# Optimization experiments

Hardware: AMD Instinct MI355X
Metric: run time of the kernel (lower is better)

## Reference

```python
import jax, jax.numpy as jnp
import numpy as np
from jax import lax

B, C, H, W = 4, 256, 32, 32   # latent: NCHW, C == codebook embed dim
N_CODES = 16384


def setup_inputs() -> dict:
    key = jax.random.key(0)
    k1, k2, k3 = jax.random.split(key, 3)
    latent = jax.random.normal(k1, (B, C, H, W), jnp.float32)
    codebook = jax.random.normal(k2, (N_CODES, C), jnp.float32)
    dec_w = jax.random.normal(k3, (3, C, 3, 3), jnp.float32) * 0.02
    dec_b = jnp.zeros((3,), jnp.float32)
    return {"latent": latent, "codebook": codebook, "dec_w": dec_w, "dec_b": dec_b}


def vector_quantize(x, codebook):
    # x: [B,H,W,D], codebook: [N,D]. Squared-L2 nearest neighbor + gather,
    # straight-through gradient (replace_grad(x_q, x)).
    d = ((x * x).sum(-1, keepdims=True)
         - 2.0 * jnp.einsum('bhwd,nd->bhwn', x, codebook)
         + (codebook * codebook).sum(-1))          # [B,H,W,N]
    idx = jnp.argmin(d, axis=-1)                    # [B,H,W]
    x_q = codebook[idx]                             # gather -> [B,H,W,D]
    return x + lax.stop_gradient(x_q - x)


@jax.custom_vjp
def clamp_with_grad(x):
    return jnp.clip(x, 0.0, 1.0)

def _cwg_fwd(x):
    return jnp.clip(x, 0.0, 1.0), x

def _cwg_bwd(x, g):
    # pass gradient only where it points back toward the valid range
    keep = (g * (x - jnp.clip(x, 0.0, 1.0)) >= 0).astype(g.dtype)
    return (g * keep,)

clamp_with_grad.defvjp(_cwg_fwd, _cwg_bwd)


def decode(quant, dec_w, dec_b):
    # stub VQGAN decoder: single 3x3 conv embed_dim -> 3 (NCHW)
    y = lax.conv_general_dilated(quant, dec_w, window_strides=(1, 1),
                                 padding='SAME',
                                 dimension_numbers=('NCHW', 'OIHW', 'NCHW'))
    return y + dec_b[None, :, None, None]


def reference(latent, codebook, dec_w, dec_b):
    x = jnp.moveaxis(latent, 1, 3)                  # NCHW -> NHWC
    quant = jnp.moveaxis(vector_quantize(x, codebook), 3, 1)  # back to NCHW
    img = decode(quant, dec_w, dec_b)
    return clamp_with_grad((img + 1.0) * 0.5)
```

## Files before the change

kernel.cpp:

```cpp
#include <hip/hip_runtime.h>
#include <hip/hip_bf16.h>
#include <stdint.h>

#define P_TOT   4096
#define N_CODE  16384
#define DIM     256
#define HW      1024
#define CHW     262144
#define NBLK    16

typedef unsigned long long u64;
typedef unsigned short u16;
typedef __attribute__((ext_vector_type(4))) float f32x4;
typedef __attribute__((ext_vector_type(8))) short bf16x8;
typedef __attribute__((ext_vector_type(8))) unsigned short ushort8;

#define FENCE() asm volatile("" ::: "memory")
#define BAR()   __builtin_amdgcn_s_barrier()
#define VM(n)   asm volatile("s_waitcnt vmcnt(" #n ")" ::: "memory")

__device__ __forceinline__ unsigned int mono(float f) {
  unsigned int u = __float_as_uint(f);
  return (u & 0x80000000u) ? ~u : (u | 0x80000000u);
}
__device__ __forceinline__ u16 f2bf(float f) {
  __hip_bfloat16 h = __float2bfloat16(f);
  return *(u16*)&h;
}
__device__ __forceinline__ float bf2f(u16 b) {
  __hip_bfloat16 h = *(__hip_bfloat16*)&b;
  return __bfloat162float(h);
}
__device__ __forceinline__ void gload16(const void* g, void* l) {
  __builtin_amdgcn_global_load_lds(
      (const __attribute__((address_space(1))) unsigned int*)g,
      (__attribute__((address_space(3))) unsigned int*)l, 16, 0, 0);
}

__global__ __launch_bounds__(256) void k_prep(const float* __restrict__ cb,
                                              const float* __restrict__ latent,
                                              const float* __restrict__ dec_w,
                                              u16* __restrict__ bfrag,
                                              u16* __restrict__ xfrag,
                                              float* __restrict__ cnorm,
                                              float* __restrict__ wt) {
  __shared__ float ls[64][68];
  int bid = blockIdx.x;
  int t = threadIdx.x;
  if (bid < 1024) {
    int blk = bid;
    int kp = blk & 3, bq = (blk >> 2) & 3, nb = blk >> 4;
    int code0 = nb * 256 + bq * 64;
    int k0 = kp * 64;
    int lr = t >> 4, lc = (t & 15) * 4;
    #pragma unroll
    for (int pss = 0; pss < 4; ++pss) {
      int row = pss * 16 + lr;
      float4 v = *(const float4*)&cb[(size_t)(code0 + row) * DIM + k0 + lc];
      ls[row][lc] = v.x; ls[row][lc + 1] = v.y; ls[row][lc + 2] = v.z; ls[row][lc + 3] = v.w;
    }
    __syncthreads();
    int row64 = t & 63, g = t >> 6;
    #pragma unroll
    for (int it = 0; it < 4; ++it) {
      int combo = it * 4 + g;
      int kt2 = combo >> 3, s = (combo >> 1) & 3, h = combo & 1;
      int kt = kp * 2 + kt2;
      ushort8 o;
      #pragma unroll
      for (int e = 0; e < 8; ++e) {
        float x = ls[row64][kt2 * 32 + s * 8 + e];
        u16 hi = f2bf(x);
        o[e] = h ? f2bf(x - bf2f(hi)) : hi;
      }
      size_t unitIdx = (size_t)(nb * 8 + kt) * 4 + bq;
      *(ushort8*)&bfrag[unitIdx * 4096 + (size_t)((h * 4 + s) * 64 + row64) * 8] = o;
    }
  } else if (bid < 1280) {
    int blk = bid - 1024;
    int kp = blk & 3, rowblk = blk >> 2;
    int g0 = rowblk * 64;
    int b = g0 >> 10, hw0 = g0 & 1023;
    int c0 = kp * 64;
    int ch = t >> 4, px4 = (t & 15) * 4;
    #pragma unroll
    for (int pss = 0; pss < 4; ++pss) {
      int c = pss * 16 + ch;
      float4 v = *(const float4*)&latent[(size_t)b * CHW + (size_t)(c0 + c) * HW + hw0 + px4];
      ls[px4 + 0][c] = v.x; ls[px4 + 1][c] = v.y; ls[px4 + 2][c] = v.z; ls[px4 + 3][c] = v.w;
    }
    __syncthreads();
    int row64 = t & 63, g = t >> 6;
    #pragma unroll
    for (int it = 0; it < 4; ++it) {
      int combo = it * 4 + g;
      int kt2 = combo >> 3, s = (combo >> 1) & 3, h = combo & 1;
      int kt = kp * 2 + kt2;
      ushort8 o;
      #pragma unroll
      for (int e = 0; e < 8; ++e) {
        float x = ls[row64][kt2 * 32 + s * 8 + e];
        u16 hi = f2bf(x);
        o[e] = h ? f2bf(x - bf2f(hi)) : hi;
      }
      int mbO = rowblk >> 2, aq = rowblk & 3;
      size_t unitIdx = (size_t)(mbO * 8 + kt) * 4 + aq;
      *(ushort8*)&xfrag[unitIdx * 4096 + (size_t)((h * 4 + s) * 64 + row64) * 8] = o;
    }
  } else if (bid < 5376) {
    int code = (bid - 1280) * 4 + (t >> 6);
    int lane = t & 63;
    float4 v = ((const float4*)(cb + (size_t)code * DIM))[lane];
    float sv = fmaf(v.x, v.x, fmaf(v.y, v.y, fmaf(v.z, v.z, v.w * v.w)));
    #pragma unroll
    for (int off = 32; off; off >>= 1) sv += __shfl_down(sv, off, 64);
    if (lane == 0) cnorm[code] = sv;
  } else {
    int e = (bid - 5376) * 256 + t;
    if (e < 6912) {
      int ic = e & 255; int r = e >> 8;
      int kx = r % 3; r /= 3; int ky = r % 3; int oc = r / 3;
      wt[e] = dec_w[((oc * 256 + ic) * 3 + ky) * 3 + kx];
    }
  }
}

__global__ __launch_bounds__(512, 2) void k_vq(const u16* __restrict__ xfrag,
                                               const u16* __restrict__ bfrag,
                                               const float* __restrict__ cnorm,
                                               u64* __restrict__ partial) {
  __shared__ u16 lds[2][2][4][4096];
  __shared__ float cnl[1024];

  int bid = blockIdx.x;
  int xcd = bid & 7, ix = bid >> 3;
  int nbc = xcd * 2 + (ix >> 4);
  int mb  = ix & 15;

  int tid = threadIdx.x, lane = tid & 63, w = tid >> 6;
  int fr = lane & 15, s = lane >> 4;
  int aq = w >> 1;
  int rbase = (w & 1) * 32;
  int tid8 = tid * 8;

  const u16* Xb = xfrag + (size_t)mb * 32 * 4096;
  const u16* Bb = bfrag + (size_t)nbc * 128 * 4096;

  cnl[tid]       = cnorm[nbc * 1024 + tid];
  cnl[tid + 512] = cnorm[nbc * 1024 + 512 + tid];
  __syncthreads();

  #pragma unroll
  for (int r = 0; r < 4; ++r) gload16(Xb + (size_t)r * 4096 + tid8, &lds[0][0][r][0] + tid8);
  #pragma unroll
  for (int r = 0; r < 4; ++r) gload16(Bb + (size_t)r * 4096 + tid8, &lds[0][1][r][0] + tid8);
  VM(0); BAR(); FENCE();

  f32x4 acc[2][16] = {};
  u64 best[4]  = {~0ull, ~0ull, ~0ull, ~0ull};
  u64 best2[4] = {~0ull, ~0ull, ~0ull, ~0ull};
  bf16x8 ah[2], al[2], bh[4], bl[4];

  #define READ_A(LA)                                                          \
    _Pragma("unroll")                                                         \
    for (int m = 0; m < 2; ++m) {                                             \
      ah[m] = *(const bf16x8*)&(LA)[aq * 4096 + (size_t)((0 + s) * 64 + rbase + m * 16 + fr) * 8]; \
      al[m] = *(const bf16x8*)&(LA)[aq * 4096 + (size_t)((4 + s) * 64 + rbase + m * 16 + fr) * 8]; \
    }
  #define READ_B(LB, q)                                                       \
    _Pragma("unroll")                                                         \
    for (int j = 0; j < 4; ++j) {                                             \
      bh[j] = *(const bf16x8*)&(LB)[(q) * 4096 + (size_t)((0 + s) * 64 + j * 16 + fr) * 8]; \
      bl[j] = *(const bf16x8*)&(LB)[(q) * 4096 + (size_t)((4 + s) * 64 + j * 16 + fr) * 8]; \
    }
  #define MFMAQ(q)                                                            \
    __builtin_amdgcn_s_setprio(1);                                            \
    _Pragma("unroll")                                                         \
    for (int m = 0; m < 2; ++m) {                                             \
      _Pragma("unroll")                                                       \
      for (int j = 0; j < 4; ++j)                                             \
        acc[m][(q) * 4 + j] = __builtin_amdgcn_mfma_f32_16x16x32_bf16(ah[m], bh[j], acc[m][(q) * 4 + j], 0, 0, 0); \
    }                                                                         \
    _Pragma("unroll")                                                         \
    for (int m = 0; m < 2; ++m) {                                             \
      _Pragma("unroll")                                                       \
      for (int j = 0; j < 4; ++j)                                             \
        acc[m][(q) * 4 + j] = __builtin_amdgcn_mfma_f32_16x16x32_bf16(ah[m], bl[j], acc[m][(q) * 4 + j], 0, 0, 0); \
    }                                                                         \
    _Pragma("unroll")                                                         \
    for (int m = 0; m < 2; ++m) {                                             \
      _Pragma("unroll")                                                       \
      for (int j = 0; j < 4; ++j)                                             \
        acc[m][(q) * 4 + j] = __builtin_amdgcn_mfma_f32_16x16x32_bf16(al[m], bh[j], acc[m][(q) * 4 + j], 0, 0, 0); \
    }                                                                         \
    __builtin_amdgcn_s_setprio(0);
  #define FOLD(pp)                                                            \
    _Pragma("unroll")                                                         \
    for (int n = 0; n < 16; ++n) {                                            \
      float cnv = cnl[(pp) * 256 + n * 16 + fr];                              \
      unsigned code = (unsigned)(nbc * 1024 + (pp) * 256 + n * 16 + fr);      \
      _Pragma("unroll")                                                       \
      for (int r = 0; r < 4; ++r) {                                           \
        float v0 = fmaf(-2.0f, acc[0][n][r], cnv);                            \
        u64 k0 = ((u64)mono(v0) << 32) | code;                                \
        if (k0 < best[r]) best[r] = k0;                                       \
        acc[0][n][r] = 0.0f;                                                  \
        float v1 = fmaf(-2.0f, acc[1][n][r], cnv);                            \
        u64 k1 = ((u64)mono(v1) << 32) | code;                                \
        if (k1 < best2[r]) best2[r] = k1;                                     \
        acc[1][n][r] = 0.0f;                                                  \
      }                                                                       \
    }

  #pragma unroll 1
  for (int tt = 0; tt < 32; ++tt) {
    const int cur = tt & 1, nxt = cur ^ 1;
    const int kt = tt & 7;
    u16* LA = &lds[cur][0][0][0];
    u16* LB = &lds[cur][1][0][0];
    const u16* SA = Xb + (size_t)((tt + 1) & 7) * 16384;
    const u16* SB = Bb + (size_t)(tt + 1) * 16384;
    const bool stage = (tt < 31);
    READ_A(LA); READ_B(LB, 0);
    if (stage) {
      #pragma unroll
      for (int r = 0; r < 4; ++r) gload16(SA + (size_t)r * 4096 + tid8, &lds[nxt][0][r][0] + tid8);
      #pragma unroll
      for (int r = 0; r < 4; ++r) gload16(SB + (size_t)r * 4096 + tid8, &lds[nxt][1][r][0] + tid8);
    }
    MFMAQ(0);
    READ_B(LB, 1);
    MFMAQ(1);
    READ_B(LB, 2);
    MFMAQ(2);
    READ_B(LB, 3);
    MFMAQ(3);
    if (kt == 7) { FOLD(tt >> 3); }
    VM(0);
    BAR(); FENCE();
  }

  #pragma unroll
  for (int d = 1; d < 16; d <<= 1) {
    #pragma unroll
    for (int r = 0; r < 4; ++r) {
      u64 o = __shfl_xor(best[r], d, 64);
      if (o < best[r]) best[r] = o;
      u64 o2 = __shfl_xor(best2[r], d, 64);
      if (o2 < best2[r]) best2[r] = o2;
    }
  }
  if (fr == 0) {
    int rowb = mb * 256 + w * 32 + s * 4;
    #pragma unroll
    for (int r = 0; r < 4; ++r) {
      partial[(size_t)(rowb + r) * NBLK + nbc] = best[r];
      partial[(size_t)(rowb + 16 + r) * NBLK + nbc] = best2[r];
    }
  }
}

__global__ __launch_bounds__(256) void k_idx(const u64* __restrict__ partial,
                                             const float* __restrict__ latent,
                                             const float* __restrict__ cb,
                                             int* __restrict__ idxo) {
  int p = (blockIdx.x * 256 + threadIdx.x) >> 6;
  int lane = threadIdx.x & 63;
  u64 v = (lane < NBLK) ? partial[(size_t)p * NBLK + lane] : ~0ull;
  u64 m1 = v;
  #pragma unroll
  for (int d = 1; d < 64; d <<= 1) { u64 o = __shfl_xor(m1, d, 64); if (o < m1) m1 = o; }
  u64 vv = (v == m1) ? ~0ull : v;
  u64 m2 = vv;
  #pragma unroll
  for (int d = 1; d < 64; d <<= 1) { u64 o = __shfl_xor(m2, d, 64); if (o < m2) m2 = o; }
  int n1 = (int)(m1 & 0xFFFFFFFFull);
  int n2 = (int)(m2 & 0xFFFFFFFFull);

  int b = p >> 10, hw = p & 1023;
  const float* xb = latent + (size_t)b * CHW + hw;
  double d1 = 0.0, d2 = 0.0;
  #pragma unroll
  for (int q = 0; q < 4; ++q) {
    int c = lane * 4 + q;
    double xv = (double)xb[(size_t)c * HW];
    double e1 = xv - (double)cb[(size_t)n1 * DIM + c]; d1 += e1 * e1;
    double e2 = xv - (double)cb[(size_t)n2 * DIM + c]; d2 += e2 * e2;
  }
  #pragma unroll
  for (int d = 32; d; d >>= 1) {
    d1 += __shfl_down(d1, d, 64);
    d2 += __shfl_down(d2, d, 64);
  }
  if (lane == 0) {
    idxo[p] = (d2 < d1 || (d2 == d1 && n2 < n1)) ? n2 : n1;
  }
}

__global__ __launch_bounds__(256) void k_conv(const int* __restrict__ idxo,
                                              const float* __restrict__ cb,
                                              const float* __restrict__ wt,
                                              const float* __restrict__ bias,
                                              float* __restrict__ out) {
  __shared__ int idxl[3][32];
  int y = blockIdx.x, b = blockIdx.y;
  int t = threadIdx.x;
  if (t < 96) {
    int r = t >> 5, px = t & 31;
    int yy = min(max(y + r - 1, 0), 31);
    idxl[r][px] = idxo[b * HW + yy * 32 + px];
  }
  __syncthreads();

  int x = t & 31, icg = t >> 5;
  float a0 = 0.f, a1 = 0.f, a2 = 0.f;
  #pragma unroll
  for (int dy = -1; dy <= 1; dy++) {
    int yy = y + dy;
    if (yy < 0 || yy >= 32) continue;
    #pragma unroll
    for (int dx = -1; dx <= 1; dx++) {
      int xx = x + dx;
      if (xx < 0 || xx >= 32) continue;
      int n = idxl[dy + 1][xx];
      const float4* crow = (const float4*)(cb + (size_t)n * DIM + icg * 32);
      int tap = (dy + 1) * 3 + (dx + 1);
      const float4* w0p = (const float4*)(wt + (size_t)(0 * 9 + tap) * DIM + icg * 32);
      const float4* w1p = (const float4*)(wt + (size_t)(1 * 9 + tap) * DIM + icg * 32);
      const float4* w2p = (const float4*)(wt + (size_t)(2 * 9 + tap) * DIM + icg * 32);
      #pragma unroll
      for (int q = 0; q < 8; q++) {
        float4 qv = crow[q];
        float4 wa = w0p[q];
        a0 = fmaf(qv.x, wa.x, a0); a0 = fmaf(qv.y, wa.y, a0);
        a0 = fmaf(qv.z, wa.z, a0); a0 = fmaf(qv.w, wa.w, a0);
        float4 wb = w1p[q];
        a1 = fmaf(qv.x, wb.x, a1); a1 = fmaf(qv.y, wb.y, a1);
        a1 = fmaf(qv.z, wb.z, a1); a1 = fmaf(qv.w, wb.w, a1);
        float4 wcv = w2p[q];
        a2 = fmaf(qv.x, wcv.x, a2); a2 = fmaf(qv.y, wcv.y, a2);
        a2 = fmaf(qv.z, wcv.z, a2); a2 = fmaf(qv.w, wcv.w, a2);
      }
    }
  }
  __shared__ float red[3][32][8];
  red[0][x][icg] = a0; red[1][x][icg] = a1; red[2][x][icg] = a2;
  __syncthreads();
  if (t < 96) {
    int oc = t >> 5, xo = t & 31;
    float sum = 0.f;
    #pragma unroll
    for (int k = 0; k < 8; k++) sum += red[oc][xo][k];
    sum += bias[oc];
    sum = (sum + 1.0f) * 0.5f;
    sum = fminf(fmaxf(sum, 0.0f), 1.0f);
    out[((size_t)(b * 3 + oc) * 32 + y) * 32 + xo] = sum;
  }
}

extern "C" void kernel_launch(void* const* d_in, const int* in_sizes, int n_in,
                              void* d_out, int out_size, void* d_ws, size_t ws_size,
                              hipStream_t stream) {
  const float* latent = (const float*)d_in[0];
  const float* cb     = (const float*)d_in[1];
  const float* dec_w  = (const float*)d_in[2];
  const float* dec_b  = (const float*)d_in[3];
  float* out = (float*)d_out;

  char* ws = (char*)d_ws;
  u64*   partial = (u64*)ws;
  float* cnorm   = (float*)(ws + 0x080000);
  int*   idx     = (int*)  (ws + 0x090000);
  float* wt      = (float*)(ws + 0x094000);
  u16*   xfrag   = (u16*)  (ws + 0x100000);
  u16*   bfrag   = (u16*)  (ws + 0x800000);

  k_prep<<<dim3(5403), dim3(256), 0, stream>>>(cb, latent, dec_w, bfrag, xfrag, cnorm, wt);
  k_vq  <<<dim3(256),  dim3(512), 0, stream>>>(xfrag, bfrag, cnorm, partial);
  k_idx <<<dim3(1024), dim3(256), 0, stream>>>(partial, latent, cb, idx);
  k_conv<<<dim3(32, 4), dim3(256), 0, stream>>>(idx, cb, wt, dec_b, out);
}
```

Baseline: 191.7 us.

## Retile VQ MFMA warps to 2x4 grid with LDS argmin reduction

```diff
diff --git a/kernel.cpp b/kernel.cpp
--- a/kernel.cpp
+++ b/kernel.cpp
@@ -42,6 +42,7 @@
                                               const float* __restrict__ dec_w,
                                               u16* __restrict__ bfrag,
                                               u16* __restrict__ xfrag,
+                                              float* __restrict__ xt,
                                               float* __restrict__ cnorm,
                                               float* __restrict__ wt) {
   __shared__ float ls[64][68];
@@ -107,6 +108,14 @@
       size_t unitIdx = (size_t)(mbO * 8 + kt) * 4 + aq;
       *(ushort8*)&xfrag[unitIdx * 4096 + (size_t)((h * 4 + s) * 64 + row64) * 8] = o;
     }
+    int pix = t >> 2, sub = t & 3;
+    #pragma unroll
+    for (int q = 0; q < 4; ++q) {
+      int c = sub * 16 + q * 4;
+      float4 v;
+      v.x = ls[pix][c]; v.y = ls[pix][c + 1]; v.z = ls[pix][c + 2]; v.w = ls[pix][c + 3];
+      *(float4*)&xt[(size_t)(g0 + pix) * DIM + c0 + c] = v;
+    }
   } else if (bid < 5376) {
     int code = (bid - 1280) * 4 + (t >> 6);
     int lane = t & 63;
@@ -131,6 +140,7 @@
                                                u64* __restrict__ partial) {
   __shared__ u16 lds[2][2][4][4096];
   __shared__ float cnl[1024];
+  __shared__ u64 red[256][4];
 
   int bid = blockIdx.x;
   int xcd = bid & 7, ix = bid >> 3;
@@ -139,8 +149,7 @@
 
   int tid = threadIdx.x, lane = tid & 63, w = tid >> 6;
   int fr = lane & 15, s = lane >> 4;
-  int aq = w >> 1;
-  int rbase = (w & 1) * 32;
+  int wr = w >> 2, wc = w & 3;
   int tid8 = tid * 8;
 
   const u16* Xb = xfrag + (size_t)mb * 32 * 4096;
@@ -148,6 +157,8 @@
 
   cnl[tid]       = cnorm[nbc * 1024 + tid];
   cnl[tid + 512] = cnorm[nbc * 1024 + 512 + tid];
+  ((u64*)red)[tid]       = ~0ull;
+  ((u64*)red)[tid + 512] = ~0ull;
   __syncthreads();
 
   #pragma unroll
@@ -156,112 +167,105 @@
   for (int r = 0; r < 4; ++r) gload16(Bb + (size_t)r * 4096 + tid8, &lds[0][1][r][0] + tid8);
   VM(0); BAR(); FENCE();
 
-  f32x4 acc[2][16] = {};
-  u64 best[4]  = {~0ull, ~0ull, ~0ull, ~0ull};
-  u64 best2[4] = {~0ull, ~0ull, ~0ull, ~0ull};
-  bf16x8 ah[2], al[2], bh[4], bl[4];
-
-  #define READ_A(LA)                                                          \
+  f32x4 acc[8][4] = {};
+
+  #define FOLD(pp) {                                                          \
+    float cnv[4]; unsigned codev[4];                                          \
     _Pragma("unroll")                                                         \
-    for (int m = 0; m < 2; ++m) {                                             \
-      ah[m] = *(const bf16x8*)&(LA)[aq * 4096 + (size_t)((0 + s) * 64 + rbase + m * 16 + fr) * 8]; \
-      al[m] = *(const bf16x8*)&(LA)[aq * 4096 + (size_t)((4 + s) * 64 + rbase + m * 16 + fr) * 8]; \
-    }
-  #define READ_B(LB, q)                                                       \
-    _Pragma("unroll")                                                         \
-    for (int j = 0; j < 4; ++j) {                                             \
-      bh[j] = *(const bf16x8*)&(LB)[(q) * 4096 + (size_t)((0 + s) * 64 + j * 16 + fr) * 8]; \
-      bl[j] = *(const bf16x8*)&(LB)[(q) * 4096 + (size_t)((4 + s) * 64 + j * 16 + fr) * 8]; \
-    }
-  #define MFMAQ(q)                                                            \
-    __builtin_amdgcn_s_setprio(1);                                            \
-    _Pragma("unroll")                                                         \
-    for (int m = 0; m < 2; ++m) {                                             \
-      _Pragma("unroll")                                                       \
-      for (int j = 0; j < 4; ++j)                                             \
-        acc[m][(q) * 4 + j] = __builtin_amdgcn_mfma_f32_16x16x32_bf16(ah[m], bh[j], acc[m][(q) * 4 + j], 0, 0, 0); \
+    for (int nf = 0; nf < 4; ++nf) {                                          \
+      cnv[nf] = cnl[(pp) * 256 + wc * 64 + nf * 16 + fr];                     \
+      codev[nf] = (unsigned)(nbc * 1024 + (pp) * 256 + wc * 64 + nf * 16 + fr); \
     }                                                                         \
     _Pragma("unroll")                                                         \
-    for (int m = 0; m < 2; ++m) {                                             \
+    for (int mfr = 0; mfr < 8; ++mfr) {                                       \
+      u64 bb[4];                                                              \
       _Pragma("unroll")                                                       \
-      for (int j = 0; j < 4; ++j)                                             \
-        acc[m][(q) * 4 + j] = __builtin_amdgcn_mfma_f32_16x16x32_bf16(ah[m], bl[j], acc[m][(q) * 4 + j], 0, 0, 0); \
+      for (int rr = 0; rr < 4; ++rr) {                                        \
+        u64 m = ~0ull;                                                        \
+        _Pragma("unroll")                                                     \
+        for (int nf = 0; nf < 4; ++nf) {                                      \
+          float val = fmaf(-2.0f, acc[mfr][nf][rr], cnv[nf]);                 \
+          u64 key = ((u64)mono(val) << 32) | codev[nf];                       \
+          if (key < m) m = key;                                               \
+        }                                                                     \
+        bb[rr] = m;                                                           \
+      }                                                                       \
+      _Pragma("unroll")                                                       \
+      for (int d = 1; d < 16; d <<= 1) {                                      \
+        _Pragma("unroll")                                                     \
+        for (int rr = 0; rr < 4; ++rr) {                                      \
+          u64 o = __shfl_xor(bb[rr], d, 64);                                  \
+          if (o < bb[rr]) bb[rr] = o;                                         \
+        }                                                                     \
+      }                                                                       \
+      if (fr == 0) {                                                          \
+        _Pragma("unroll")                                                     \
+        for (int rr = 0; rr < 4; ++rr) {                                      \
+          int row = wr * 128 + mfr * 16 + s * 4 + rr;                         \
+          u64 old = red[row][wc];                                             \
+          red[row][wc] = (bb[rr] < old) ? bb[rr] : old;                       \
+        }                                                                     \
+      }                                                                       \
+      _Pragma("unroll")                                                       \
+      for (int nf = 0; nf < 4; ++nf)                                          \
+        _Pragma("unroll")                                                     \
+        for (int rr = 0; rr < 4; ++rr) acc[mfr][nf][rr] = 0.0f;               \
     }                                                                         \
-    _Pragma("unroll")                                                         \
-    for (int m = 0; m < 2; ++m) {                                             \
-      _Pragma("unroll")                                                       \
-      for (int j = 0; j < 4; ++j)                                             \
-        acc[m][(q) * 4 + j] = __builtin_amdgcn_mfma_f32_16x16x32_bf16(al[m], bh[j], acc[m][(q) * 4 + j], 0, 0, 0); \
-    }                                                                         \
-    __builtin_amdgcn_s_setprio(0);
-  #define FOLD(pp)                                                            \
-    _Pragma("unroll")                                                         \
-    for (int n = 0; n < 16; ++n) {                                            \
-      float cnv = cnl[(pp) * 256 + n * 16 + fr];                              \
-      unsigned code = (unsigned)(nbc * 1024 + (pp) * 256 + n * 16 + fr);      \
-      _Pragma("unroll")                                                       \
-      for (int r = 0; r < 4; ++r) {                                           \
-        float v0 = fmaf(-2.0f, acc[0][n][r], cnv);                            \
-        u64 k0 = ((u64)mono(v0) << 32) | code;                                \
-        if (k0 < best[r]) best[r] = k0;                                       \
-        acc[0][n][r] = 0.0f;                                                  \
-        float v1 = fmaf(-2.0f, acc[1][n][r], cnv);                            \
-        u64 k1 = ((u64)mono(v1) << 32) | code;                                \
-        if (k1 < best2[r]) best2[r] = k1;                                     \
-        acc[1][n][r] = 0.0f;                                                  \
-      }                                                                       \
-    }
+  }
 
   #pragma unroll 1
   for (int tt = 0; tt < 32; ++tt) {
     const int cur = tt & 1, nxt = cur ^ 1;
     const int kt = tt & 7;
-    u16* LA = &lds[cur][0][0][0];
-    u16* LB = &lds[cur][1][0][0];
-    const u16* SA = Xb + (size_t)((tt + 1) & 7) * 16384;
-    const u16* SB = Bb + (size_t)(tt + 1) * 16384;
-    const bool stage = (tt < 31);
-    READ_A(LA); READ_B(LB, 0);
-    if (stage) {
+    const u16* LA = &lds[cur][0][0][0];
+    const u16* LB = &lds[cur][1][0][0];
+    if (tt < 31) {
+      const u16* SA = Xb + (size_t)((tt + 1) & 7) * 16384;
+      const u16* SB = Bb + (size_t)(tt + 1) * 16384;
       #pragma unroll
       for (int r = 0; r < 4; ++r) gload16(SA + (size_t)r * 4096 + tid8, &lds[nxt][0][r][0] + tid8);
       #pragma unroll
       for (int r = 0; r < 4; ++r) gload16(SB + (size_t)r * 4096 + tid8, &lds[nxt][1][r][0] + tid8);
     }
-    MFMAQ(0);
-    READ_B(LB, 1);
-    MFMAQ(1);
-    READ_B(LB, 2);
-    MFMAQ(2);
-    READ_B(LB, 3);
-    MFMAQ(3);
+    bf16x8 bh[4], bl[4];
+    #pragma unroll
+    for (int nf = 0; nf < 4; ++nf) {
+      bh[nf] = *(const bf16x8*)&LB[wc * 4096 + (size_t)((0 + s) * 64 + nf * 16 + fr) * 8];
+      bl[nf] = *(const bf16x8*)&LB[wc * 4096 + (size_t)((4 + s) * 64 + nf * 16 + fr) * 8];
+    }
+    #pragma unroll
+    for (int mfr = 0; mfr < 8; ++mfr) {
+      const int au = wr * 2 + (mfr >> 2);
+      const int r64 = (mfr & 3) * 16 + fr;
+      bf16x8 ah = *(const bf16x8*)&LA[au * 4096 + (size_t)((0 + s) * 64 + r64) * 8];
+      bf16x8 al = *(const bf16x8*)&LA[au * 4096 + (size_t)((4 + s) * 64 + r64) * 8];
+      __builtin_amdgcn_s_setprio(1);
+      #pragma unroll
+      for (int nf = 0; nf < 4; ++nf)
+        acc[mfr][nf] = __builtin_amdgcn_mfma_f32_16x16x32_bf16(ah, bh[nf], acc[mfr][nf], 0, 0, 0);
+      #pragma unroll
+      for (int nf = 0; nf < 4; ++nf)
+        acc[mfr][nf] = __builtin_amdgcn_mfma_f32_16x16x32_bf16(ah, bl[nf], acc[mfr][nf], 0, 0, 0);
+      #pragma unroll
+      for (int nf = 0; nf < 4; ++nf)
+        acc[mfr][nf] = __builtin_amdgcn_mfma_f32_16x16x32_bf16(al, bh[nf], acc[mfr][nf], 0, 0, 0);
+      __builtin_amdgcn_s_setprio(0);
+    }
     if (kt == 7) { FOLD(tt >> 3); }
     VM(0);
     BAR(); FENCE();
   }
 
-  #pragma unroll
-  for (int d = 1; d < 16; d <<= 1) {
-    #pragma unroll
-    for (int r = 0; r < 4; ++r) {
-      u64 o = __shfl_xor(best[r], d, 64);
-      if (o < best[r]) best[r] = o;
-      u64 o2 = __shfl_xor(best2[r], d, 64);
-      if (o2 < best2[r]) best2[r] = o2;
-    }
-  }
-  if (fr == 0) {
-    int rowb = mb * 256 + w * 32 + s * 4;
-    #pragma unroll
-    for (int r = 0; r < 4; ++r) {
-      partial[(size_t)(rowb + r) * NBLK + nbc] = best[r];
-      partial[(size_t)(rowb + 16 + r) * NBLK + nbc] = best2[r];
-    }
+  if (tid < 256) {
+    u64 m0 = red[tid][0], m1 = red[tid][1], m2 = red[tid][2], m3 = red[tid][3];
+    u64 a = m0 < m1 ? m0 : m1;
+    u64 b2 = m2 < m3 ? m2 : m3;
+    partial[(size_t)(mb * 256 + tid) * NBLK + nbc] = a < b2 ? a : b2;
   }
 }
 
 __global__ __launch_bounds__(256) void k_idx(const u64* __restrict__ partial,
-                                             const float* __restrict__ latent,
+                                             const float* __restrict__ xt,
                                              const float* __restrict__ cb,
                                              int* __restrict__ idxo) {
   int p = (blockIdx.x * 256 + threadIdx.x) >> 6;
@@ -277,15 +281,19 @@
   int n1 = (int)(m1 & 0xFFFFFFFFull);
   int n2 = (int)(m2 & 0xFFFFFFFFull);
 
-  int b = p >> 10, hw = p & 1023;
-  const float* xb = latent + (size_t)b * CHW + hw;
-  double d1 = 0.0, d2 = 0.0;
-  #pragma unroll
-  for (int q = 0; q < 4; ++q) {
-    int c = lane * 4 + q;
-    double xv = (double)xb[(size_t)c * HW];
-    double e1 = xv - (double)cb[(size_t)n1 * DIM + c]; d1 += e1 * e1;
-    double e2 = xv - (double)cb[(size_t)n2 * DIM + c]; d2 += e2 * e2;
+  float4 xv = *(const float4*)&xt[(size_t)p * DIM + lane * 4];
+  float4 ca = *(const float4*)&cb[(size_t)n1 * DIM + lane * 4];
+  float4 cbv = *(const float4*)&cb[(size_t)n2 * DIM + lane * 4];
+  double d1, d2;
+  {
+    double e0 = (double)xv.x - (double)ca.x, e1 = (double)xv.y - (double)ca.y;
+    double e2 = (double)xv.z - (double)ca.z, e3 = (double)xv.w - (double)ca.w;
+    d1 = e0 * e0 + e1 * e1 + e2 * e2 + e3 * e3;
+  }
+  {
+    double e0 = (double)xv.x - (double)cbv.x, e1 = (double)xv.y - (double)cbv.y;
+    double e2 = (double)xv.z - (double)cbv.z, e3 = (double)xv.w - (double)cbv.w;
+    d2 = e0 * e0 + e1 * e1 + e2 * e2 + e3 * e3;
   }
   #pragma unroll
   for (int d = 32; d; d >>= 1) {
@@ -374,9 +382,10 @@
   float* wt      = (float*)(ws + 0x094000);
   u16*   xfrag   = (u16*)  (ws + 0x100000);
   u16*   bfrag   = (u16*)  (ws + 0x800000);
-
-  k_prep<<<dim3(5403), dim3(256), 0, stream>>>(cb, latent, dec_w, bfrag, xfrag, cnorm, wt);
+  float* xt      = (float*)(ws + 0x1800000);
+
+  k_prep<<<dim3(5403), dim3(256), 0, stream>>>(cb, latent, dec_w, bfrag, xfrag, xt, cnorm, wt);
   k_vq  <<<dim3(256),  dim3(512), 0, stream>>>(xfrag, bfrag, cnorm, partial);
-  k_idx <<<dim3(1024), dim3(256), 0, stream>>>(partial, latent, cb, idx);
+  k_idx <<<dim3(1024), dim3(256), 0, stream>>>(partial, xt, cb, idx);
   k_conv<<<dim3(32, 4), dim3(256), 0, stream>>>(idx, cb, wt, dec_b, out);
 }
```

New measurement: 206.4 us. +7.6%, slower.
